# Performance work log

Measured on AMD Instinct MI355X. Metric: run time of the kernel, lower is better.

## Reference

```python
import jax, jax.numpy as jnp
import numpy as np

N_NODES = 100000
N_EDGES = 1600000
IN_CH = 128
HID = 64
HEADS = 2
OUT_CH = 2
EDGE_DIM = 3
NEG_SLOPE = 0.2
EPS = 1e-16  # PyG softmax denominator epsilon


def gat_conv(x, edge_index, edge_attr, W, We, att_src, att_dst, att_edge, bias, heads, out_ch, concat):
    """Faithful PyG GATConv (edge_dim enabled, eval mode, add_self_loops handled by caller=False here
    since the repo passes raw edge_index; PyG default add_self_loops=True is intentionally mirrored below)."""
    N = x.shape[0]
    src, dst = edge_index[0], edge_index[1]
    H, C = heads, out_ch
    h = (x @ W).reshape(N, H, C)                    # [N,H,C] node projections
    e = (edge_attr @ We).reshape(-1, H, C)          # [E,H,C] edge projections
    a_src = jnp.sum(h * att_src, axis=-1)           # [N,H]
    a_dst = jnp.sum(h * att_dst, axis=-1)           # [N,H]
    alpha = a_src[src] + a_dst[dst] + jnp.sum(e * att_edge, axis=-1)  # [E,H]
    alpha = jax.nn.leaky_relu(alpha, NEG_SLOPE)
    # segment softmax over incoming edges of each dst node
    amax = jax.ops.segment_max(alpha, dst, num_segments=N)            # [N,H]
    amax = jnp.where(jnp.isfinite(amax), amax, 0.0)
    alpha = jnp.exp(alpha - amax[dst])
    denom = jax.ops.segment_sum(alpha, dst, num_segments=N)           # [N,H]
    alpha = alpha / (denom[dst] + EPS)
    msg = h[src] * alpha[:, :, None]                                  # [E,H,C]
    out = jax.ops.segment_sum(msg, dst, num_segments=N)               # [N,H,C]
    if concat:
        out = out.reshape(N, H * C)
    else:
        out = out.mean(axis=1)
    return out + bias


def add_self_loops(edge_index, edge_attr, n):
    loops = jnp.arange(n, dtype=edge_index.dtype)
    ei = jnp.concatenate([edge_index, jnp.stack([loops, loops])], axis=1)
    ea = jnp.concatenate([edge_attr, jnp.zeros((n, edge_attr.shape[1]), edge_attr.dtype)], axis=0)
    return ei, ea


def setup_inputs() -> dict:
    key = jax.random.key(0)
    ks = jax.random.split(key, 16)
    s = 0.1
    x = jax.random.normal(ks[0], (N_NODES, IN_CH), jnp.float32)
    edge_index = jax.random.randint(ks[1], (2, N_EDGES), 0, N_NODES, jnp.int64 if jax.config.jax_enable_x64 else jnp.int32)
    edge_feat = jax.random.normal(ks[2], (N_EDGES, EDGE_DIM), jnp.float32)
    HC = HEADS * HID
    return {
        "x": x, "edge_index": edge_index, "edge_feat": edge_feat,
        "W1": jax.random.normal(ks[3], (IN_CH, HC), jnp.float32) * s,
        "We1": jax.random.normal(ks[4], (EDGE_DIM, HC), jnp.float32) * s,
        "as1": jax.random.normal(ks[5], (1, HEADS, HID), jnp.float32) * s,
        "ad1": jax.random.normal(ks[6], (1, HEADS, HID), jnp.float32) * s,
        "ae1": jax.random.normal(ks[7], (1, HEADS, HID), jnp.float32) * s,
        "b1": jnp.zeros((HC,), jnp.float32),
        "W2": jax.random.normal(ks[8], (HC, OUT_CH), jnp.float32) * s,
        "We2": jax.random.normal(ks[9], (EDGE_DIM, OUT_CH), jnp.float32) * s,
        "as2": jax.random.normal(ks[10], (1, 1, OUT_CH), jnp.float32) * s,
        "ad2": jax.random.normal(ks[11], (1, 1, OUT_CH), jnp.float32) * s,
        "ae2": jax.random.normal(ks[12], (1, 1, OUT_CH), jnp.float32) * s,
        "b2": jnp.zeros((OUT_CH,), jnp.float32),
    }


def reference(x, edge_index, edge_feat, W1, We1, as1, ad1, ae1, b1, W2, We2, as2, ad2, ae2, b2):
    # eval mode: F.dropout is identity
    ei, ea = add_self_loops(edge_index, edge_feat, x.shape[0])  # PyG GATConv default add_self_loops=True
    h = gat_conv(x, ei, ea, W1, We1, as1, ad1, ae1, b1, HEADS, HID, concat=True)
    h = jax.nn.elu(h)
    out = gat_conv(h, ei, ea, W2, We2, as2, ad2, ae2, b2, 1, OUT_CH, concat=False)
    return out
```

## Files before the change

kernel.cpp:

```cpp
#include <hip/hip_runtime.h>
#include <hip/hip_bf16.h>

#define NN 100000
#define NE 1600000
#define NEG_SLOPE 0.2f
#define GEPS 1e-16f
#define WSHIFT 4.0f

#define HB 32
#define EB (NE / HB)
#define HPASS 4
#define HBIN 25000
#define HBW (HBIN / 2)
#define CAPS ((size_t)(NE + 8 * NN))

typedef __attribute__((ext_vector_type(8))) short short8;
typedef __attribute__((ext_vector_type(4))) float f32x4;
typedef __attribute__((ext_vector_type(2))) _Float16 h2v;

__device__ __forceinline__ unsigned short f2b(float f) {
  unsigned u = __float_as_uint(f);
  u += 0x7fffu + ((u >> 16) & 1u);
  return (unsigned short)(u >> 16);
}
__device__ __forceinline__ unsigned short f2h(float f) {
  _Float16 h = (_Float16)f;
  return __builtin_bit_cast(unsigned short, h);
}
__device__ __forceinline__ float h2f(unsigned short u) {
  return (float)__builtin_bit_cast(_Float16, u);
}
__device__ __forceinline__ unsigned pkh2(float lo, float hi) {
  return (unsigned)f2h(lo) | ((unsigned)f2h(hi) << 16);
}
__device__ __forceinline__ float dot2h(unsigned a, unsigned b, float c) {
  return __builtin_amdgcn_fdot2(__builtin_bit_cast(h2v, a), __builtin_bit_cast(h2v, b), c, false);
}
__device__ __forceinline__ unsigned permb(unsigned s0, unsigned s1, int sel) {
  return __builtin_amdgcn_perm(s0, s1, sel);
}
#define HSEL_LO 0x05040100
#define HSEL_HI 0x07060302
#define ONE2    0x3C003C00u
#define EZPAD   (-60000.0f)

__global__ void k_prep(const float* __restrict__ We1, const float* __restrict__ ae1,
                       const float* __restrict__ We2, const float* __restrict__ ae2,
                       const float* __restrict__ W1, const float* __restrict__ as1,
                       const float* __restrict__ ad1,
                       float* __restrict__ q, float4* __restrict__ pq) {
  int t = threadIdx.x;
  if (t < 6) {
    int d = t >> 1, hh = t & 1;
    float s = 0.f;
    for (int c = 0; c < 64; ++c) s += We1[d * 128 + hh * 64 + c] * ae1[hh * 64 + c];
    q[t] = s;
  } else if (t < 9) {
    int d = t - 6;
    q[8 + d] = We2[d * 2 + 0] * ae2[0] + We2[d * 2 + 1] * ae2[1];
  }
  if (t < 128) {
    float s0 = 0.f, s1 = 0.f, d0 = 0.f, d1 = 0.f;
    for (int c = 0; c < 64; ++c) {
      float w0 = W1[t * 128 + c], w1 = W1[t * 128 + 64 + c];
      s0 += w0 * as1[c];      s1 += w1 * as1[64 + c];
      d0 += w0 * ad1[c];      d1 += w1 * ad1[64 + c];
    }
    pq[t] = make_float4(s0, s1, d0, d1);
  }
}

__global__ __launch_bounds__(512, 4) void k_gemm(const float* __restrict__ x,
                                                 const float* __restrict__ W,
                                                 const float4* __restrict__ pq,
                                                 unsigned short* __restrict__ h1b,
                                                 float* __restrict__ a1s,
                                                 float* __restrict__ a1d) {
  __shared__ unsigned short xa[128 * 128];
  __shared__ unsigned short wt[128 * 128];
  int t = threadIdx.x;
  int row0 = blockIdx.x * 128;

  {
    int kr = t >> 2, n0 = (t & 3) * 32;
    const float* wp = &W[kr * 128 + n0];
    int cb = kr >> 3, klo = kr & 7;
#pragma unroll
    for (int j = 0; j < 8; ++j) {
      float4 v = *(const float4*)&wp[j * 4];
      int n = n0 + j * 4;
      wt[(n + 0) * 128 + ((cb ^ ((n + 0) & 15)) * 8) + klo] = f2b(v.x);
      wt[(n + 1) * 128 + ((cb ^ ((n + 1) & 15)) * 8) + klo] = f2b(v.y);
      wt[(n + 2) * 128 + ((cb ^ ((n + 2) & 15)) * 8) + klo] = f2b(v.z);
      wt[(n + 3) * 128 + ((cb ^ ((n + 3) & 15)) * 8) + klo] = f2b(v.w);
    }
  }
  {
    int lrow = t >> 2, qq = t & 3;
    int grow = row0 + lrow; if (grow >= NN) grow = NN - 1;
    const float* xp = &x[(size_t)grow * 128 + qq * 32];
    const float4* pqp = &pq[qq * 32];
    float ps0 = 0.f, ps1 = 0.f, pd0 = 0.f, pd1 = 0.f;
    int sw = lrow & 15;
#pragma unroll
    for (int j = 0; j < 4; ++j) {
      float4 u = *(const float4*)&xp[j * 8];
      float4 v = *(const float4*)&xp[j * 8 + 4];
      float xs[8] = {u.x, u.y, u.z, u.w, v.x, v.y, v.z, v.w};
      short8 sv;
#pragma unroll
      for (int e = 0; e < 8; ++e) {
        float4 pv = pqp[j * 8 + e];
        ps0 += xs[e] * pv.x; ps1 += xs[e] * pv.y;
        pd0 += xs[e] * pv.z; pd1 += xs[e] * pv.w;
        sv[e] = (short)f2b(xs[e]);
      }
      int c = qq * 4 + j;
      *(short8*)&xa[lrow * 128 + ((c ^ sw) * 8)] = sv;
    }
    ps0 += __shfl_xor(ps0, 1); ps0 += __shfl_xor(ps0, 2);
    ps1 += __shfl_xor(ps1, 1); ps1 += __shfl_xor(ps1, 2);
    pd0 += __shfl_xor(pd0, 1); pd0 += __shfl_xor(pd0, 2);
    pd1 += __shfl_xor(pd1, 1); pd1 += __shfl_xor(pd1, 2);
    if (qq == 0) {
      *(float2*)&a1s[grow * 2] = make_float2(ps0, ps1);
      *(float2*)&a1d[grow * 2] = make_float2(pd0, pd1);
    }
  }
  __syncthreads();

  int lane = t & 63, w = t >> 6;
  int m = lane & 15, quad = lane >> 4;
  int wm = (w & 1) * 64, wn = (w >> 1) * 32;
  f32x4 acc[4][2];
#pragma unroll
  for (int mi = 0; mi < 4; ++mi)
#pragma unroll
    for (int ni = 0; ni < 2; ++ni) acc[mi][ni] = (f32x4)(0.f);

#pragma unroll
  for (int kk = 0; kk < 4; ++kk) {
    int c = kk * 4 + quad;
    int co = (c ^ m) * 8;
    short8 a[4], b[2];
#pragma unroll
    for (int mi = 0; mi < 4; ++mi)
      a[mi] = *(const short8*)&xa[(wm + mi * 16 + m) * 128 + co];
#pragma unroll
    for (int ni = 0; ni < 2; ++ni)
      b[ni] = *(const short8*)&wt[(wn + ni * 16 + m) * 128 + co];
#pragma unroll
    for (int mi = 0; mi < 4; ++mi)
#pragma unroll
      for (int ni = 0; ni < 2; ++ni)
        acc[mi][ni] = __builtin_amdgcn_mfma_f32_16x16x32_bf16(a[mi], b[ni], acc[mi][ni], 0, 0, 0);
  }
#pragma unroll
  for (int mi = 0; mi < 4; ++mi)
#pragma unroll
    for (int r = 0; r < 4; ++r) {
      int grow = row0 + wm + mi * 16 + quad * 4 + r;
      if (grow >= NN) grow = NN - 1;
#pragma unroll
      for (int ni = 0; ni < 2; ++ni)
        h1b[(size_t)grow * 128 + wn + ni * 16 + m] = f2h(acc[mi][ni][r]);
    }
}

__global__ __launch_bounds__(1024) void k_hist(const int* __restrict__ ei,
                                               unsigned short* __restrict__ off16,
                                               unsigned short* __restrict__ rank) {
  __shared__ unsigned cnt[HBW];
  int b = blockIdx.x >> 2;
  int pass = blockIdx.x & 3;
  int base = pass * HBIN;
  int t = threadIdx.x;
  for (int i = t; i < HBW; i += 1024) cnt[i] = 0;
  __syncthreads();
  const int* dsts = &ei[NE + b * EB];
  for (int i = t * 4; i < EB; i += 4096) {
    int4 d = *(const int4*)&dsts[i];
    int dv[4] = {d.x, d.y, d.z, d.w};
#pragma unroll
    for (int j = 0; j < 4; ++j) {
      int rel = dv[j] - base;
      if ((unsigned)rel < (unsigned)HBIN) {
        unsigned sh = (unsigned)(rel & 1) << 4;
        unsigned old = atomicAdd(&cnt[rel >> 1], 1u << sh);
        rank[b * EB + i + j] = (unsigned short)((old >> sh) & 0xffffu);
      }
    }
  }
  __syncthreads();
  unsigned short* dp = &off16[(size_t)b * NN + base];
  for (int i = t; i < HBW; i += 1024) *(unsigned*)&dp[i * 2] = cnt[i];
}

__global__ void k_sumdeg(unsigned short* __restrict__ off16, int* __restrict__ deg) {
  int n = blockIdx.x * 256 + threadIdx.x;
  if (n >= NN) return;
  int run = 0;
#pragma unroll
  for (int b = 0; b < HB; ++b) {
    size_t idx = (size_t)b * NN + n;
    int c = off16[idx];
    off16[idx] = (unsigned short)run;
    run += c;
  }
  deg[n] = run;
}

__device__ __forceinline__ int padlen(int d) { return (d + 8) & ~7; }

__global__ void k_scan1(const int* __restrict__ deg, int* __restrict__ bsum) {
  __shared__ int lds[256];
  int t = threadIdx.x;
  int base = blockIdx.x * 1024 + t * 4;
  int s = 0;
  for (int j = 0; j < 4; ++j) { int i = base + j; s += (i < NN) ? padlen(deg[i]) : 0; }
  lds[t] = s; __syncthreads();
  for (int o = 128; o > 0; o >>= 1) { if (t < o) lds[t] += lds[t + o]; __syncthreads(); }
  if (t == 0) bsum[blockIdx.x] = lds[0];
}

__global__ void k_scan2(int* __restrict__ bsum, int nb) {
  __shared__ int lds[128];
  int t = threadIdx.x;
  int v = (t < nb) ? bsum[t] : 0;
  lds[t] = v; __syncthreads();
  for (int o = 1; o < 128; o <<= 1) {
    int u = (t >= o) ? lds[t - o] : 0;
    __syncthreads();
    lds[t] += u;
    __syncthreads();
  }
  if (t < nb) bsum[t] = lds[t] - v;
}

__global__ void k_scan3(const int* __restrict__ deg, const int* __restrict__ bbase,
                        const float* __restrict__ a1s, const float* __restrict__ a1d,
                        int* __restrict__ rowptr, float2* __restrict__ cpk1,
                        unsigned short* __restrict__ ezh) {
  __shared__ int lds[256];
  int t = threadIdx.x;
  int base = blockIdx.x * 1024 + t * 4;
  int v[4]; int s = 0;
  for (int j = 0; j < 4; ++j) { int i = base + j; v[j] = (i < NN) ? padlen(deg[i]) : 0; s += v[j]; }
  lds[t] = s; __syncthreads();
  for (int o = 1; o < 256; o <<= 1) {
    int u = (t >= o) ? lds[t - o] : 0;
    __syncthreads();
    lds[t] += u;
    __syncthreads();
  }
  int excl = lds[t] - s + bbase[blockIdx.x];
  unsigned short ezpad = f2h(EZPAD);
  for (int j = 0; j < 4; ++j) {
    int i = base + j;
    if (i <= NN) rowptr[i] = excl;
    if (i < NN) {
      float al0 = a1s[i * 2] + a1d[i * 2];
      float al1 = a1s[i * 2 + 1] + a1d[i * 2 + 1];
      al0 = al0 > 0.f ? al0 : NEG_SLOPE * al0;
      al1 = al1 > 0.f ? al1 : NEG_SLOPE * al1;
      cpk1[excl] = make_float2(
          __uint_as_float(pkh2(__expf(al0 - WSHIFT), __expf(al1 - WSHIFT))),
          __int_as_float(i));
      ezh[excl] = 0;
      float2 pad = make_float2(0.f, __int_as_float(i));
      for (int k = 1 + deg[i]; k < v[j]; ++k) { cpk1[excl + k] = pad; ezh[excl + k] = ezpad; }
    }
    excl += v[j];
  }
}

__global__ void k_scatter(const int* __restrict__ ei, const float* __restrict__ ef,
                          const float* __restrict__ a1s, const float* __restrict__ a1d,
                          const float* __restrict__ q, const int* __restrict__ rowptr,
                          const unsigned short* __restrict__ rank,
                          const unsigned short* __restrict__ off16,
                          float2* __restrict__ cpk1, unsigned short* __restrict__ ezh) {
  int t4 = blockIdx.x * 256 + threadIdx.x;
  if (t4 >= NE / 4) return;
  int e0 = t4 * 4;
  int hb = e0 / EB;
  const unsigned short* offp = &off16[(size_t)hb * NN];
  int4 ss = *(const int4*)&ei[e0];
  int4 dd = *(const int4*)&ei[NE + e0];
  ushort4 rk = *(const ushort4*)&rank[e0];
  float4 fA = *(const float4*)&ef[e0 * 3];
  float4 fB = *(const float4*)&ef[e0 * 3 + 4];
  float4 fC = *(const float4*)&ef[e0 * 3 + 8];
  float f[4][3] = {{fA.x, fA.y, fA.z}, {fA.w, fB.x, fB.y},
                   {fB.z, fB.w, fC.x}, {fC.y, fC.z, fC.w}};
  int src[4] = {ss.x, ss.y, ss.z, ss.w};
  int dst[4] = {dd.x, dd.y, dd.z, dd.w};
  int rnk[4] = {rk.x, rk.y, rk.z, rk.w};
#pragma unroll
  for (int j = 0; j < 4; ++j) {
    float e0h = f[j][0] * q[0] + f[j][1] * q[2] + f[j][2] * q[4];
    float e1h = f[j][0] * q[1] + f[j][1] * q[3] + f[j][2] * q[5];
    float ez  = f[j][0] * q[8] + f[j][1] * q[9] + f[j][2] * q[10];
    float al0 = a1s[src[j] * 2] + a1d[dst[j] * 2] + e0h;
    float al1 = a1s[src[j] * 2 + 1] + a1d[dst[j] * 2 + 1] + e1h;
    al0 = al0 > 0.f ? al0 : NEG_SLOPE * al0;
    al1 = al1 > 0.f ? al1 : NEG_SLOPE * al1;
    int pos = rowptr[dst[j]] + 1 + (int)offp[dst[j]] + rnk[j];
    cpk1[pos] = make_float2(
        __uint_as_float(pkh2(__expf(al0 - WSHIFT), __expf(al1 - WSHIFT))),
        __int_as_float(src[j]));
    ezh[pos] = f2h(ez);
  }
}

__global__ __launch_bounds__(256) void k_agg1(const unsigned short* __restrict__ h1b,
                                              const int* __restrict__ rowptr,
                                              const float2* __restrict__ cpk1,
                                              const float* __restrict__ b1,
                                              const float* __restrict__ W2,
                                              const float* __restrict__ as2,
                                              const float* __restrict__ ad2,
                                              float4* __restrict__ nd) {
  int n = (int)((blockIdx.x * 256 + threadIdx.x) >> 6);
  int lane = threadIdx.x & 63;
  if (n >= NN) return;
  int s0 = rowptr[n], s1 = rowptr[n + 1];
  int g = lane >> 4;
  int lp = lane & 15;
  int wsel = (lp >= 8) ? HSEL_HI : HSEL_LO;

  float acc[8];
#pragma unroll
  for (int j = 0; j < 8; ++j) acc[j] = 0.f;
  float den = 0.f;

  int i = s0;
  for (; i + 16 <= s1; i += 16) {
    const float4* pp = (const float4*)(cpk1 + i + 4 * g);
    float4 p01 = pp[0];
    float4 p23 = pp[1];
    uint4 vA = *((const uint4*)(h1b + ((size_t)__float_as_int(p01.y) << 7)) + lp);
    uint4 vB = *((const uint4*)(h1b + ((size_t)__float_as_int(p01.w) << 7)) + lp);
    uint4 vC = *((const uint4*)(h1b + ((size_t)__float_as_int(p23.y) << 7)) + lp);
    uint4 vD = *((const uint4*)(h1b + ((size_t)__float_as_int(p23.w) << 7)) + lp);
    unsigned wAB = permb(__float_as_uint(p01.z), __float_as_uint(p01.x), wsel);
    unsigned wCD = permb(__float_as_uint(p23.z), __float_as_uint(p23.x), wsel);
    den = dot2h(wAB, ONE2, den);
    den = dot2h(wCD, ONE2, den);
    acc[0] = dot2h(permb(vB.x, vA.x, HSEL_LO), wAB, acc[0]);
    acc[1] = dot2h(permb(vB.x, vA.x, HSEL_HI), wAB, acc[1]);
    acc[2] = dot2h(permb(vB.y, vA.y, HSEL_LO), wAB, acc[2]);
    acc[3] = dot2h(permb(vB.y, vA.y, HSEL_HI), wAB, acc[3]);
    acc[4] = dot2h(permb(vB.z, vA.z, HSEL_LO), wAB, acc[4]);
    acc[5] = dot2h(permb(vB.z, vA.z, HSEL_HI), wAB, acc[5]);
    acc[6] = dot2h(permb(vB.w, vA.w, HSEL_LO), wAB, acc[6]);
    acc[7] = dot2h(permb(vB.w, vA.w, HSEL_HI), wAB, acc[7]);
    acc[0] = dot2h(permb(vD.x, vC.x, HSEL_LO), wCD, acc[0]);
    acc[1] = dot2h(permb(vD.x, vC.x, HSEL_HI), wCD, acc[1]);
    acc[2] = dot2h(permb(vD.y, vC.y, HSEL_LO), wCD, acc[2]);
    acc[3] = dot2h(permb(vD.y, vC.y, HSEL_HI), wCD, acc[3]);
    acc[4] = dot2h(permb(vD.z, vC.z, HSEL_LO), wCD, acc[4]);
    acc[5] = dot2h(permb(vD.z, vC.z, HSEL_HI), wCD, acc[5]);
    acc[6] = dot2h(permb(vD.w, vC.w, HSEL_LO), wCD, acc[6]);
    acc[7] = dot2h(permb(vD.w, vC.w, HSEL_HI), wCD, acc[7]);
  }
  if (i < s1) {
    float4 p = *(const float4*)(cpk1 + i + 2 * g);
    uint4 vA = *((const uint4*)(h1b + ((size_t)__float_as_int(p.y) << 7)) + lp);
    uint4 vB = *((const uint4*)(h1b + ((size_t)__float_as_int(p.w) << 7)) + lp);
    unsigned wAB = permb(__float_as_uint(p.z), __float_as_uint(p.x), wsel);
    den = dot2h(wAB, ONE2, den);
    acc[0] = dot2h(permb(vB.x, vA.x, HSEL_LO), wAB, acc[0]);
    acc[1] = dot2h(permb(vB.x, vA.x, HSEL_HI), wAB, acc[1]);
    acc[2] = dot2h(permb(vB.y, vA.y, HSEL_LO), wAB, acc[2]);
    acc[3] = dot2h(permb(vB.y, vA.y, HSEL_HI), wAB, acc[3]);
    acc[4] = dot2h(permb(vB.z, vA.z, HSEL_LO), wAB, acc[4]);
    acc[5] = dot2h(permb(vB.z, vA.z, HSEL_HI), wAB, acc[5]);
    acc[6] = dot2h(permb(vB.w, vA.w, HSEL_LO), wAB, acc[6]);
    acc[7] = dot2h(permb(vB.w, vA.w, HSEL_HI), wAB, acc[7]);
  }
#pragma unroll
  for (int o = 16; o <= 32; o <<= 1) {
    den += __shfl_xor(den, o);
#pragma unroll
    for (int j = 0; j < 8; ++j) acc[j] += __shfl_xor(acc[j], o);
  }
  float4 bA = *(const float4*)&b1[lp * 8];
  float4 bB = *(const float4*)&b1[lp * 8 + 4];
  float bb[8] = {bA.x, bA.y, bA.z, bA.w, bB.x, bB.y, bB.z, bB.w};
  float inv = 1.f / (den + GEPS);
  float r[8];
#pragma unroll
  for (int j = 0; j < 8; ++j) {
    float v = acc[j] * inv + bb[j];
    r[j] = v > 0.f ? v : __expf(v) - 1.f;
  }
  float4 wA = *(const float4*)&W2[lp * 16];
  float4 wB = *(const float4*)&W2[lp * 16 + 4];
  float4 wC = *(const float4*)&W2[lp * 16 + 8];
  float4 wD = *(const float4*)&W2[lp * 16 + 12];
  float p20 = r[0] * wA.x + r[1] * wA.z + r[2] * wB.x + r[3] * wB.z
            + r[4] * wC.x + r[5] * wC.z + r[6] * wD.x + r[7] * wD.z;
  float p21 = r[0] * wA.y + r[1] * wA.w + r[2] * wB.y + r[3] * wB.w
            + r[4] * wC.y + r[5] * wC.w + r[6] * wD.y + r[7] * wD.w;
#pragma unroll
  for (int o = 1; o <= 8; o <<= 1) { p20 += __shfl_xor(p20, o); p21 += __shfl_xor(p21, o); }
  if (lane == 0) {
    float4 v;
    v.x = p20; v.y = p21;
    v.z = p20 * as2[0] + p21 * as2[1];
    v.w = p20 * ad2[0] + p21 * ad2[1];
    nd[n] = v;
  }
}

__global__ __launch_bounds__(256) void k_agg2(const int* __restrict__ rowptr,
                                              const float2* __restrict__ cpk1,
                                              const unsigned short* __restrict__ ezh,
                                              const float4* __restrict__ nd,
                                              const float* __restrict__ b2,
                                              float* __restrict__ out) {
  int wid = (int)((blockIdx.x * 256 + threadIdx.x) >> 6);
  int lane = threadIdx.x & 63;
  int g = lane >> 4, lp = lane & 15;
  int n = wid * 4 + g;
  if (n >= NN) return;
  int s0 = rowptr[n], s1 = rowptr[n + 1];
  float adn = nd[n].w;
  float den = 0.f, acc0 = 0.f, acc1 = 0.f;
  for (int i = s0 + lp; i < s1; i += 16) {
    float2 pk = cpk1[i];
    float ezv = h2f(ezh[i]);
    int s = __float_as_int(pk.y);
    float4 ns = nd[s];
    float v = ns.z + adn + ezv;
    v = v > 0.f ? v : NEG_SLOPE * v;
    float p = __expf(v);
    den += p;
    acc0 += p * ns.x;
    acc1 += p * ns.y;
  }
#pragma unroll
  for (int o = 1; o <= 8; o <<= 1) {
    den += __shfl_xor(den, o);
    acc0 += __shfl_xor(acc0, o);
    acc1 += __shfl_xor(acc1, o);
  }
  if (lp == 0) {
    float2 r;
    r.x = acc0 / (den + GEPS) + b2[0];
    r.y = acc1 / (den + GEPS) + b2[1];
    *(float2*)&out[n * 2] = r;
  }
}

extern "C" void kernel_launch(void* const* d_in, const int* in_sizes, int n_in,
                              void* d_out, int out_size, void* d_ws, size_t ws_size,
                              hipStream_t stream) {
  (void)in_sizes; (void)n_in; (void)out_size; (void)ws_size;
  const float* x   = (const float*)d_in[0];
  const int*   ei  = (const int*)d_in[1];
  const float* ef  = (const float*)d_in[2];
  const float* W1  = (const float*)d_in[3];
  const float* We1 = (const float*)d_in[4];
  const float* as1 = (const float*)d_in[5];
  const float* ad1 = (const float*)d_in[6];
  const float* ae1 = (const float*)d_in[7];
  const float* b1  = (const float*)d_in[8];
  const float* W2  = (const float*)d_in[9];
  const float* We2 = (const float*)d_in[10];
  const float* as2 = (const float*)d_in[11];
  const float* ad2 = (const float*)d_in[12];
  const float* ae2 = (const float*)d_in[13];
  const float* b2  = (const float*)d_in[14];
  float* out = (float*)d_out;

  char* w = (char*)d_ws;
  auto alloc = [&](size_t bytes) -> char* {
    char* p = w; w += (bytes + 255) & ~(size_t)255; return p;
  };
  unsigned short* h1b = (unsigned short*)alloc((size_t)NN * 128 * 2);
  float*  a1s    = (float*)alloc((size_t)NN * 2 * 4);
  float*  a1d    = (float*)alloc((size_t)NN * 2 * 4);
  float4* nd     = (float4*)alloc((size_t)NN * 16);
  float*  q      = (float*)alloc(64);
  float4* pq     = (float4*)alloc(128 * 16);
  int*    deg    = (int*)alloc((size_t)NN * 4);
  int*    rowptr = (int*)alloc((size_t)(NN + 1) * 4);
  unsigned short* rank  = (unsigned short*)alloc((size_t)NE * 2);
  unsigned short* off16 = (unsigned short*)alloc((size_t)HB * NN * 2);
  int*    bsum   = (int*)alloc(128 * 4);
  float2* cpk1   = (float2*)alloc(CAPS * 8);
  unsigned short* ezh = (unsigned short*)alloc(CAPS * 2);

  const int NB_SCAN = (NN + 1023) / 1024;

  hipLaunchKernelGGL(k_prep, dim3(1), dim3(128), 0, stream,
                     We1, ae1, We2, ae2, W1, as1, ad1, q, pq);
  hipLaunchKernelGGL(k_gemm, dim3((NN + 127) / 128), dim3(512), 0, stream,
                     x, W1, pq, h1b, a1s, a1d);
  hipLaunchKernelGGL(k_hist, dim3(HB * HPASS), dim3(1024), 0, stream, ei, off16, rank);
  hipLaunchKernelGGL(k_sumdeg, dim3((NN + 255) / 256), dim3(256), 0, stream, off16, deg);
  hipLaunchKernelGGL(k_scan1, dim3(NB_SCAN), dim3(256), 0, stream, deg, bsum);
  hipLaunchKernelGGL(k_scan2, dim3(1), dim3(128), 0, stream, bsum, NB_SCAN);
  hipLaunchKernelGGL(k_scan3, dim3(NB_SCAN), dim3(256), 0, stream,
                     deg, bsum, a1s, a1d, rowptr, cpk1, ezh);
  hipLaunchKernelGGL(k_scatter, dim3((NE / 4 + 255) / 256), dim3(256), 0, stream,
                     ei, ef, a1s, a1d, q, rowptr, rank, off16, cpk1, ezh);
  hipLaunchKernelGGL(k_agg1, dim3((NN * 64 + 255) / 256), dim3(256), 0, stream,
                     h1b, rowptr, cpk1, b1, W2, as2, ad2, nd);
  hipLaunchKernelGGL(k_agg2, dim3(((NN + 3) / 4 * 64 + 255) / 256), dim3(256), 0, stream,
                     rowptr, cpk1, ezh, nd, b2, out);
}
```

Baseline: 380.9 us.

## Replace random CSR scatter with two-phase bucketed binning through staging buffers

The single random-write scatter kernel becomes a two-pass scheme run over each half of the edges. The first pass computes edge weights, bins edges by destination bucket in LDS and writes them to staging arrays with per-block bucket offsets. The second pass has one block per bucket replay those staged entries, so writes to cpk1/ezh land in a narrow address range and get better cache locality. The cost is extra staging traffic, four launches instead of one, and a mostly serial per-thread loop in the second pass.

```diff
diff --git a/kernel.cpp b/kernel.cpp
--- a/kernel.cpp
+++ b/kernel.cpp
@@ -13,6 +13,13 @@
 #define HBIN 25000
 #define HBW (HBIN / 2)
 #define CAPS ((size_t)(NE + 8 * NN))
+
+#define BKN  250
+#define NBUK 400
+#define EHALF (NE / 2)
+#define ABLK 1000
+#define NAB (EHALF / ABLK)
+#define BSTR (NBUK + 4)
 
 typedef __attribute__((ext_vector_type(8))) short short8;
 typedef __attribute__((ext_vector_type(4))) float f32x4;
@@ -274,42 +281,105 @@
   }
 }
 
-__global__ void k_scatter(const int* __restrict__ ei, const float* __restrict__ ef,
-                          const float* __restrict__ a1s, const float* __restrict__ a1d,
-                          const float* __restrict__ q, const int* __restrict__ rowptr,
-                          const unsigned short* __restrict__ rank,
-                          const unsigned short* __restrict__ off16,
-                          float2* __restrict__ cpk1, unsigned short* __restrict__ ezh) {
-  int t4 = blockIdx.x * 256 + threadIdx.x;
-  if (t4 >= NE / 4) return;
-  int e0 = t4 * 4;
-  int hb = e0 / EB;
-  const unsigned short* offp = &off16[(size_t)hb * NN];
-  int4 ss = *(const int4*)&ei[e0];
-  int4 dd = *(const int4*)&ei[NE + e0];
-  ushort4 rk = *(const ushort4*)&rank[e0];
-  float4 fA = *(const float4*)&ef[e0 * 3];
-  float4 fB = *(const float4*)&ef[e0 * 3 + 4];
-  float4 fC = *(const float4*)&ef[e0 * 3 + 8];
-  float f[4][3] = {{fA.x, fA.y, fA.z}, {fA.w, fB.x, fB.y},
-                   {fB.z, fB.w, fC.x}, {fC.y, fC.z, fC.w}};
-  int src[4] = {ss.x, ss.y, ss.z, ss.w};
-  int dst[4] = {dd.x, dd.y, dd.z, dd.w};
-  int rnk[4] = {rk.x, rk.y, rk.z, rk.w};
-#pragma unroll
-  for (int j = 0; j < 4; ++j) {
-    float e0h = f[j][0] * q[0] + f[j][1] * q[2] + f[j][2] * q[4];
-    float e1h = f[j][0] * q[1] + f[j][1] * q[3] + f[j][2] * q[5];
-    float ez  = f[j][0] * q[8] + f[j][1] * q[9] + f[j][2] * q[10];
-    float al0 = a1s[src[j] * 2] + a1d[dst[j] * 2] + e0h;
-    float al1 = a1s[src[j] * 2 + 1] + a1d[dst[j] * 2 + 1] + e1h;
-    al0 = al0 > 0.f ? al0 : NEG_SLOPE * al0;
-    al1 = al1 > 0.f ? al1 : NEG_SLOPE * al1;
-    int pos = rowptr[dst[j]] + 1 + (int)offp[dst[j]] + rnk[j];
-    cpk1[pos] = make_float2(
-        __uint_as_float(pkh2(__expf(al0 - WSHIFT), __expf(al1 - WSHIFT))),
-        __int_as_float(src[j]));
-    ezh[pos] = f2h(ez);
+__global__ __launch_bounds__(256) void k_binA(
+    const int* __restrict__ ei, const float* __restrict__ ef,
+    const float* __restrict__ a1s, const float* __restrict__ a1d,
+    const float* __restrict__ q, const int* __restrict__ rowptr,
+    const unsigned short* __restrict__ rank, const unsigned short* __restrict__ off16,
+    int half,
+    int* __restrict__ stagP, unsigned* __restrict__ stagW,
+    int* __restrict__ stagS, unsigned short* __restrict__ stagE,
+    unsigned short* __restrict__ bstart) {
+  __shared__ unsigned scnt[NBUK];
+  __shared__ unsigned sA[NBUK], sB[NBUK];
+  __shared__ int ldsP[ABLK];
+  __shared__ unsigned ldsW[ABLK];
+  __shared__ int ldsS[ABLK];
+  __shared__ unsigned short ldsE[ABLK];
+  int c = blockIdx.x, t = threadIdx.x;
+  for (int i = t; i < NBUK; i += 256) scnt[i] = 0;
+  __syncthreads();
+
+  int posr[4]; unsigned w01r[4]; int srcr[4]; unsigned short ezr[4];
+  int bkr[4]; unsigned lrkr[4];
+  bool act = t < (ABLK / 4);
+  if (act) {
+    int le0 = c * ABLK + t * 4;
+    int e0 = half * EHALF + le0;
+    int hb = e0 / EB;
+    const unsigned short* offp = &off16[(size_t)hb * NN];
+    int4 ss = *(const int4*)&ei[e0];
+    int4 dd = *(const int4*)&ei[NE + e0];
+    ushort4 rk = *(const ushort4*)&rank[e0];
+    float4 fA = *(const float4*)&ef[(size_t)e0 * 3];
+    float4 fB = *(const float4*)&ef[(size_t)e0 * 3 + 4];
+    float4 fC = *(const float4*)&ef[(size_t)e0 * 3 + 8];
+    float f[4][3] = {{fA.x, fA.y, fA.z}, {fA.w, fB.x, fB.y},
+                     {fB.z, fB.w, fC.x}, {fC.y, fC.z, fC.w}};
+    int src[4] = {ss.x, ss.y, ss.z, ss.w};
+    int dst[4] = {dd.x, dd.y, dd.z, dd.w};
+    int rnk[4] = {rk.x, rk.y, rk.z, rk.w};
+#pragma unroll
+    for (int j = 0; j < 4; ++j) {
+      float e0h = f[j][0] * q[0] + f[j][1] * q[2] + f[j][2] * q[4];
+      float e1h = f[j][0] * q[1] + f[j][1] * q[3] + f[j][2] * q[5];
+      float ez  = f[j][0] * q[8] + f[j][1] * q[9] + f[j][2] * q[10];
+      float al0 = a1s[src[j] * 2] + a1d[dst[j] * 2] + e0h;
+      float al1 = a1s[src[j] * 2 + 1] + a1d[dst[j] * 2 + 1] + e1h;
+      al0 = al0 > 0.f ? al0 : NEG_SLOPE * al0;
+      al1 = al1 > 0.f ? al1 : NEG_SLOPE * al1;
+      posr[j] = rowptr[dst[j]] + 1 + (int)offp[dst[j]] + rnk[j];
+      w01r[j] = pkh2(__expf(al0 - WSHIFT), __expf(al1 - WSHIFT));
+      srcr[j] = src[j];
+      ezr[j]  = f2h(ez);
+      bkr[j]  = dst[j] / BKN;
+      lrkr[j] = atomicAdd(&scnt[bkr[j]], 1u);
+    }
+  }
+  __syncthreads();
+  for (int i = t; i < NBUK; i += 256) sA[i] = scnt[i];
+  __syncthreads();
+  unsigned* sp = sA; unsigned* dp = sB;
+  for (int off = 1; off < NBUK; off <<= 1) {
+    for (int i = t; i < NBUK; i += 256)
+      dp[i] = sp[i] + ((i >= off) ? sp[i - off] : 0u);
+    __syncthreads();
+    unsigned* tmp = sp; sp = dp; dp = tmp;
+  }
+  for (int i = t; i <= NBUK; i += 256) {
+    unsigned v = (i == 0) ? 0u : sp[i - 1];
+    bstart[(size_t)c * BSTR + i] = (unsigned short)v;
+  }
+  if (act) {
+#pragma unroll
+    for (int j = 0; j < 4; ++j) {
+      unsigned p = (sp[bkr[j]] - scnt[bkr[j]]) + lrkr[j];
+      ldsP[p] = posr[j]; ldsW[p] = w01r[j]; ldsS[p] = srcr[j]; ldsE[p] = ezr[j];
+    }
+  }
+  __syncthreads();
+  for (int i = t; i < ABLK; i += 256) {
+    size_t g = (size_t)c * ABLK + i;
+    stagP[g] = ldsP[i]; stagW[g] = ldsW[i]; stagS[g] = ldsS[i]; stagE[g] = ldsE[i];
+  }
+}
+
+__global__ __launch_bounds__(256) void k_binB(
+    const int* __restrict__ stagP, const unsigned* __restrict__ stagW,
+    const int* __restrict__ stagS, const unsigned short* __restrict__ stagE,
+    const unsigned short* __restrict__ bstart,
+    float2* __restrict__ cpk1, unsigned short* __restrict__ ezh) {
+  int bk = blockIdx.x, t = threadIdx.x;
+  for (int c = t; c < NAB; c += 256) {
+    const unsigned short* bs = &bstart[(size_t)c * BSTR];
+    int s = bs[bk], e2 = bs[bk + 1];
+    int base = c * ABLK;
+    for (int i = s; i < e2; ++i) {
+      int pos = stagP[base + i];
+      cpk1[pos] = make_float2(__uint_as_float(stagW[base + i]),
+                              __int_as_float(stagS[base + i]));
+      ezh[pos] = stagE[base + i];
+    }
   }
 }
 
@@ -492,6 +562,11 @@
   int*    bsum   = (int*)alloc(128 * 4);
   float2* cpk1   = (float2*)alloc(CAPS * 8);
   unsigned short* ezh = (unsigned short*)alloc(CAPS * 2);
+  int*      stagP = (int*)alloc((size_t)EHALF * 4);
+  unsigned* stagW = (unsigned*)alloc((size_t)EHALF * 4);
+  int*      stagS = (int*)alloc((size_t)EHALF * 4);
+  unsigned short* stagE = (unsigned short*)alloc((size_t)EHALF * 2);
+  unsigned short* bstart = (unsigned short*)alloc((size_t)NAB * BSTR * 2);
 
   const int NB_SCAN = (NN + 1023) / 1024;
 
@@ -505,8 +580,13 @@
   hipLaunchKernelGGL(k_scan2, dim3(1), dim3(128), 0, stream, bsum, NB_SCAN);
   hipLaunchKernelGGL(k_scan3, dim3(NB_SCAN), dim3(256), 0, stream,
                      deg, bsum, a1s, a1d, rowptr, cpk1, ezh);
-  hipLaunchKernelGGL(k_scatter, dim3((NE / 4 + 255) / 256), dim3(256), 0, stream,
-                     ei, ef, a1s, a1d, q, rowptr, rank, off16, cpk1, ezh);
+  for (int half = 0; half < 2; ++half) {
+    hipLaunchKernelGGL(k_binA, dim3(NAB), dim3(256), 0, stream,
+                       ei, ef, a1s, a1d, q, rowptr, rank, off16, half,
+                       stagP, stagW, stagS, stagE, bstart);
+    hipLaunchKernelGGL(k_binB, dim3(NBUK), dim3(256), 0, stream,
+                       stagP, stagW, stagS, stagE, bstart, cpk1, ezh);
+  }
   hipLaunchKernelGGL(k_agg1, dim3((NN * 64 + 255) / 256), dim3(256), 0, stream,
                      h1b, rowptr, cpk1, b1, W2, as2, ad2, nd);
   hipLaunchKernelGGL(k_agg2, dim3(((NN + 3) / 4 * 64 + 255) / 256), dim3(256), 0, stream,
```

After: 411.3 us. 1.08x slower.
